# Performance work log

Measured on AMD Instinct MI355X. Metric: run time of the kernel, lower is better.

## Reference

```python
import jax, jax.numpy as jnp
import numpy as np

B, S, D, H, L, OUT = 4, 1024, 1024, 16, 6, 512
HD = D // H
EPS = 1e-5


def _positional_encoding(seq, dim):
    pos = np.arange(seq, dtype=np.float32)[:, None]          # [S,1]
    i = np.arange(0, dim, 2, dtype=np.float32)[None, :]       # even indices
    div = np.power(10000.0, 2.0 * i / dim)                    # repo's (nonstandard) exponent
    pe = np.zeros((seq, dim), dtype=np.float32)
    pe[:, 0::2] = np.sin(pos / div)
    pe[:, 1::2] = np.cos(pos / div)
    return jnp.asarray(pe)[None]                               # [1,S,D]


def _causal_mask(seq):
    r = jnp.arange(seq)
    m = jnp.where(r[None, :] > r[:, None], jnp.float32(-jnp.inf), jnp.float32(0.0))
    return m[None, None]                                       # [1,1,S,S]


def setup_inputs() -> dict:
    key = jax.random.key(0)
    ks = jax.random.split(key, 10)
    sc = 0.02
    inp = {
        'x':      jax.random.normal(ks[0], (B, S, D), jnp.float32),
        'pe':     _positional_encoding(S, D),
        'mask':   _causal_mask(S),
        'ln1_g':  jnp.ones((L, D), jnp.float32),
        'ln1_b':  jnp.zeros((L, D), jnp.float32),
        'wq':     jax.random.normal(ks[1], (L, D, D), jnp.float32) * sc,
        'wk':     jax.random.normal(ks[2], (L, D, D), jnp.float32) * sc,
        'wv':     jax.random.normal(ks[3], (L, D, D), jnp.float32) * sc,
        'wo':     jax.random.normal(ks[4], (L, D, D), jnp.float32) * sc,
        'ln2_g':  jnp.ones((L, D), jnp.float32),
        'ln2_b':  jnp.zeros((L, D), jnp.float32),
        'wf':     jax.random.normal(ks[5], (L, D, D), jnp.float32) * sc,
        'lnf_g':  jnp.ones((D,), jnp.float32),
        'lnf_b':  jnp.zeros((D,), jnp.float32),
        'w_out':  jax.random.normal(ks[6], (OUT, D), jnp.float32) * sc,
    }
    return inp


def _layer_norm(x, g, b):
    mu = jnp.mean(x, axis=-1, keepdims=True)
    var = jnp.mean(jnp.square(x - mu), axis=-1, keepdims=True)
    return (x - mu) * jax.lax.rsqrt(var + EPS) * g + b


def _split_heads(x):
    b, s, d = x.shape
    return x.reshape(b, s, H, HD).transpose(0, 2, 1, 3)  # [B,H,S,HD]


def reference(x, pe, mask, ln1_g, ln1_b, wq, wk, wv, wo, ln2_g, ln2_b, wf, lnf_g, lnf_b, w_out):
    h = x + pe
    scale = 1.0 / jnp.sqrt(jnp.float32(HD))
    for l in range(wq.shape[0]):
        h_ = _layer_norm(h, ln1_g[l], ln1_b[l])
        q = _split_heads(jnp.einsum('bsd,ed->bse', h_, wq[l]))
        k = _split_heads(jnp.einsum('bsd,ed->bse', h_, wk[l]))
        v = _split_heads(jnp.einsum('bsd,ed->bse', h_, wv[l]))
        scores = jnp.einsum('bhqd,bhkd->bhqk', q, k) * scale + mask  # [B,H,S,S]
        probs = jax.nn.softmax(scores, axis=-1)
        attn = jnp.einsum('bhqk,bhkd->bhqd', probs, v)
        attn = attn.transpose(0, 2, 1, 3).reshape(h.shape)            # combine heads
        h = h + jnp.einsum('bsd,ed->bse', attn, wo[l])
        h_ = _layer_norm(h, ln2_g[l], ln2_b[l])
        h = h + jnp.einsum('bsd,ed->bse', h_, wf[l])                  # FFN = plain linear (no activation, as in source)
    h = _layer_norm(h, lnf_g, lnf_b)
    return jnp.einsum('bsd,od->bso', h, w_out)
```

## Files before the change

kernel.cpp:

```cpp
#include <hip/hip_runtime.h>
#include <hip/hip_bf16.h>
#include <stdint.h>

#define BATCH 4
#define SEQ   1024
#define DIM   1024
#define NH    16
#define HDIM  64
#define NLAYER 6
#define NOUT  512
#define NTOK  (BATCH*SEQ)
#define LOG2E 1.44269504088896f
#define NEG_BIG (-1e30f)
#define VTS   72

using bf16 = __hip_bfloat16;
typedef __attribute__((ext_vector_type(4))) float f32x4;
typedef __attribute__((ext_vector_type(8))) short bf16x8;

typedef __attribute__((address_space(1))) void as1_void;
typedef __attribute__((address_space(3))) void as3_void;

__device__ __forceinline__ float bf2f(short u) {
  union { unsigned int i; float f; } c;
  c.i = ((unsigned int)(unsigned short)u) << 16;
  return c.f;
}

__device__ __forceinline__ short f2bs(float f) {
  bf16 h = __float2bfloat16(f);
  return *(short*)&h;
}

__device__ __forceinline__ float exp_clamped(float x) {
  return exp2f(fmaxf(x, -100.f) * LOG2E);
}

__device__ __forceinline__ float loadf(const void* p, size_t i, bool f32) {
  return f32 ? ((const float*)p)[i] : __bfloat162float(((const bf16*)p)[i]);
}

__device__ __forceinline__ void g2l16(const void* g, void* l) {
  __builtin_amdgcn_global_load_lds((const as1_void*)g, (as3_void*)l, 16, 0, 0);
}

__global__ void sniff(const unsigned int* __restrict__ w, int* __restrict__ flag) {
  const int lane = threadIdx.x;
  const unsigned int word = w[lane];
  const int e2 = (word >> 7) & 0xFF;
  const bool bf16ish = (e2 >= 0x60) && (e2 <= 0x8F);
  const unsigned long long m = __ballot(bf16ish);
  if (lane == 0) *flag = (__popcll(m) >= 48) ? 0 : 1;
}

__global__ __launch_bounds__(256) void convert_all(
    const float* __restrict__ s0, const float* __restrict__ s1,
    const float* __restrict__ s2, const float* __restrict__ s3,
    const float* __restrict__ s4, const float* __restrict__ s5,
    bf16* __restrict__ d0, bf16* __restrict__ d1, bf16* __restrict__ d2,
    bf16* __restrict__ d3, bf16* __restrict__ d4, bf16* __restrict__ d5,
    const int* __restrict__ flag) {
  if (*flag == 0) return;
  int b = blockIdx.x;
  const float* s; bf16* d;
  if      (b <  768) { s = s0; d = d0; }
  else if (b < 1536) { s = s1; d = d1; b -= 768; }
  else if (b < 2304) { s = s2; d = d2; b -= 1536; }
  else if (b < 3072) { s = s3; d = d3; b -= 2304; }
  else if (b < 3840) { s = s4; d = d4; b -= 3072; }
  else               { s = s5; d = d5; b -= 3840; }
  const size_t e0 = ((size_t)b * 1024 + threadIdx.x) * 8;
  f32x4 a[4], c[4];
#pragma unroll
  for (int i = 0; i < 4; ++i) {
    a[i] = *(const f32x4*)(s + e0 + i * 2048);
    c[i] = *(const f32x4*)(s + e0 + i * 2048 + 4);
  }
#pragma unroll
  for (int i = 0; i < 4; ++i) {
    bf16x8 o;
    o[0] = f2bs(a[i][0]); o[1] = f2bs(a[i][1]); o[2] = f2bs(a[i][2]); o[3] = f2bs(a[i][3]);
    o[4] = f2bs(c[i][0]); o[5] = f2bs(c[i][1]); o[6] = f2bs(c[i][2]); o[7] = f2bs(c[i][3]);
    *(bf16x8*)(d + e0 + i * 2048) = o;
  }
}

__device__ __forceinline__ bf16x8 rd_frag(const short* panel, int row, int quad) {
  const int g  = row >> 1;
  const int cc = (((row & 1) << 2) | quad) ^ (g & 7);
  return *(const bf16x8*)(panel + g * 64 + cc * 8);
}

template<int EPI>
__device__ __forceinline__ void gemm_body(const bf16* __restrict__ A,
                                          const bf16* __restrict__ W,
                                          void* __restrict__ C,
                                          const int* __restrict__ flag,
                                          int N, int m0, int n0) {
  __shared__ __align__(16) short lA[8192];
  __shared__ __align__(16) short lB[8192];
  const int tid  = threadIdx.x;
  const int wave = tid >> 6;
  const int lane = tid & 63;
  const int quad = lane >> 4;
  const int l16  = lane & 15;
  const int wm = (wave >> 1) * 64;
  const int wn = (wave & 1) * 64;
  const int K = DIM;

  const int c3   = (lane & 7) ^ (lane >> 3);
  const int sq   = (c3 & 3) * 8;
  const int rsub = ((lane >> 3) << 1) | (c3 >> 2);
  const int ldsW = wave * 512;

  bool f32out = false;
  if (EPI == 2) f32out = (*flag != 0);

  f32x4 acc[4][4];
#pragma unroll
  for (int i = 0; i < 4; ++i)
#pragma unroll
    for (int j = 0; j < 4; ++j) acc[i][j] = (f32x4){0.f, 0.f, 0.f, 0.f};

  for (int k0 = 0; k0 < K; k0 += 64) {
    __syncthreads();
#pragma unroll
    for (int kc = 0; kc < 2; ++kc)
#pragma unroll
      for (int c = 0; c < 2; ++c) {
        const int row = c * 64 + wave * 16 + rsub;
        g2l16(A + (size_t)(m0 + row) * K + k0 + kc * 32 + sq,
              lA + kc * 4096 + c * 2048 + ldsW);
        g2l16(W + (size_t)(n0 + row) * K + k0 + kc * 32 + sq,
              lB + kc * 4096 + c * 2048 + ldsW);
      }
    __builtin_amdgcn_s_waitcnt(0);
    __syncthreads();

#pragma unroll
    for (int kc = 0; kc < 2; ++kc) {
      const short* pA = lA + kc * 4096;
      const short* pB = lB + kc * 4096;
      bf16x8 af[4], bfr[4];
#pragma unroll
      for (int i = 0; i < 4; ++i) {
        af[i]  = rd_frag(pA, wm + i * 16 + l16, quad);
        bfr[i] = rd_frag(pB, wn + i * 16 + l16, quad);
      }
#pragma unroll
      for (int i = 0; i < 4; ++i)
#pragma unroll
        for (int j = 0; j < 4; ++j)
          acc[i][j] = __builtin_amdgcn_mfma_f32_16x16x32_bf16(af[i], bfr[j], acc[i][j], 0, 0, 0);
    }
  }

#pragma unroll
  for (int i = 0; i < 4; ++i) {
    const int rowb = m0 + wm + i * 16 + quad * 4;
#pragma unroll
    for (int j = 0; j < 4; ++j) {
      const int col = n0 + wn + j * 16 + l16;
#pragma unroll
      for (int r = 0; r < 4; ++r) {
        const size_t idx = (size_t)(rowb + r) * N + col;
        const float v = acc[i][j][r];
        if (EPI == 0) ((bf16*)C)[idx] = __float2bfloat16(v);
        else { if (f32out) ((float*)C)[idx] = v; else ((bf16*)C)[idx] = __float2bfloat16(v); }
      }
    }
  }
}

__global__ __launch_bounds__(256) void gemm_out(const bf16* __restrict__ A,
                                                const bf16* __restrict__ Wc,
                                                const bf16* __restrict__ Wo,
                                                void* __restrict__ C,
                                                const int* __restrict__ flag) {
  const bf16* W = (*flag != 0) ? Wc : Wo;
  gemm_body<2>(A, W, C, flag, NOUT, blockIdx.y * 128, blockIdx.x * 128);
}

__global__ __launch_bounds__(256) void gemm_qkv(const bf16* __restrict__ A,
                                                const bf16* __restrict__ cq,
                                                const bf16* __restrict__ ck,
                                                const bf16* __restrict__ cvv,
                                                const bf16* __restrict__ oq,
                                                const bf16* __restrict__ ok,
                                                const bf16* __restrict__ ov,
                                                bf16* __restrict__ q,
                                                bf16* __restrict__ k,
                                                bf16* __restrict__ v,
                                                const int* __restrict__ flag) {
  const int gx = blockIdx.x;
  const int sel = gx >> 3;
  const int n0 = (gx & 7) * 128;
  const bool f32 = (*flag != 0);
  const bf16* W = (sel == 0) ? (f32 ? cq : oq)
                 : (sel == 1) ? (f32 ? ck : ok)
                              : (f32 ? cvv : ov);
  bf16* C = (sel == 0) ? q : (sel == 1 ? k : v);
  gemm_body<0>(A, W, C, nullptr, DIM, blockIdx.y * 128, n0);
}

__device__ __forceinline__ void gemm64_body(const bf16* __restrict__ A,
                                            const bf16* __restrict__ W,
                                            float* __restrict__ C,
                                            int N, int m0, int n0) {
  __shared__ __align__(16) short lA[4096];
  __shared__ __align__(16) short lB[8192];
  const int tid  = threadIdx.x;
  const int wave = tid >> 6;
  const int lane = tid & 63;
  const int quad = lane >> 4;
  const int l16  = lane & 15;
  const int wm = (wave >> 1) * 32;
  const int wn = (wave & 1) * 64;
  const int K = DIM;

  const int c3   = (lane & 7) ^ (lane >> 3);
  const int sq   = (c3 & 3) * 8;
  const int rsub = ((lane >> 3) << 1) | (c3 >> 2);
  const int ldsW = wave * 512;

  f32x4 acc[2][4];
#pragma unroll
  for (int i = 0; i < 2; ++i)
#pragma unroll
    for (int j = 0; j < 4; ++j) acc[i][j] = (f32x4){0.f, 0.f, 0.f, 0.f};

  for (int k0 = 0; k0 < K; k0 += 64) {
    __syncthreads();
#pragma unroll
    for (int kc = 0; kc < 2; ++kc) {
      const int arow = wave * 16 + rsub;
      g2l16(A + (size_t)(m0 + arow) * K + k0 + kc * 32 + sq,
            lA + kc * 2048 + ldsW);
#pragma unroll
      for (int c = 0; c < 2; ++c) {
        const int brow = c * 64 + wave * 16 + rsub;
        g2l16(W + (size_t)(n0 + brow) * K + k0 + kc * 32 + sq,
              lB + kc * 4096 + c * 2048 + ldsW);
      }
    }
    __builtin_amdgcn_s_waitcnt(0);
    __syncthreads();

#pragma unroll
    for (int kc = 0; kc < 2; ++kc) {
      const short* pA = lA + kc * 2048;
      const short* pB = lB + kc * 4096;
      bf16x8 af[2], bfr[4];
#pragma unroll
      for (int i = 0; i < 2; ++i)
        af[i] = rd_frag(pA, wm + i * 16 + l16, quad);
#pragma unroll
      for (int j = 0; j < 4; ++j)
        bfr[j] = rd_frag(pB, wn + j * 16 + l16, quad);
#pragma unroll
      for (int i = 0; i < 2; ++i)
#pragma unroll
        for (int j = 0; j < 4; ++j)
          acc[i][j] = __builtin_amdgcn_mfma_f32_16x16x32_bf16(af[i], bfr[j], acc[i][j], 0, 0, 0);
    }
  }

#pragma unroll
  for (int i = 0; i < 2; ++i) {
    const int rowb = m0 + wm + i * 16 + quad * 4;
#pragma unroll
    for (int j = 0; j < 4; ++j) {
      const int col = n0 + wn + j * 16 + l16;
#pragma unroll
      for (int r = 0; r < 4; ++r)
        C[(size_t)(rowb + r) * N + col] += acc[i][j][r];
    }
  }
}

__global__ __launch_bounds__(256) void gemm_add(const bf16* __restrict__ A,
                                                const bf16* __restrict__ Wc,
                                                const bf16* __restrict__ Wo,
                                                const int* __restrict__ flag,
                                                float* __restrict__ C) {
  const bf16* W = (*flag != 0) ? Wc : Wo;
  gemm64_body(A, W, C, DIM, blockIdx.y * 64, blockIdx.x * 128);
}

__global__ __launch_bounds__(256) void add_pe(const void* __restrict__ x,
                                              const void* __restrict__ pe,
                                              float* __restrict__ h,
                                              const int* __restrict__ flag) {
  const bool f32 = (*flag != 0);
  const size_t i = (size_t)blockIdx.x * 256 + threadIdx.x;
  h[i] = loadf(x, i, f32) + loadf(pe, i & (SEQ * DIM - 1), f32);
}

__global__ __launch_bounds__(256) void layernorm(const float* __restrict__ x,
                                                 const void* __restrict__ g,
                                                 const void* __restrict__ b,
                                                 int loff,
                                                 bf16* __restrict__ y,
                                                 const int* __restrict__ flag) {
  const bool f32 = (*flag != 0);
  const int row = blockIdx.x;
  const int tid = threadIdx.x;
  const int wave = tid >> 6;
  const float* xr = x + (size_t)row * DIM;
  __shared__ float red[8];

  float v[4];
  float s = 0.f;
#pragma unroll
  for (int i = 0; i < 4; ++i) { v[i] = xr[tid + 256 * i]; s += v[i]; }
#pragma unroll
  for (int off = 32; off >= 1; off >>= 1) s += __shfl_xor(s, off);
  if ((tid & 63) == 0) red[wave] = s;
  __syncthreads();
  const float mu = (red[0] + red[1] + red[2] + red[3]) * (1.f / DIM);

  float vs = 0.f;
#pragma unroll
  for (int i = 0; i < 4; ++i) { const float d = v[i] - mu; vs += d * d; }
#pragma unroll
  for (int off = 32; off >= 1; off >>= 1) vs += __shfl_xor(vs, off);
  if ((tid & 63) == 0) red[4 + wave] = vs;
  __syncthreads();
  const float var = (red[4] + red[5] + red[6] + red[7]) * (1.f / DIM);
  const float rs = rsqrtf(var + 1e-5f);

#pragma unroll
  for (int i = 0; i < 4; ++i) {
    const int d = tid + 256 * i;
    const float gv = loadf(g, (size_t)loff + d, f32);
    const float bv = loadf(b, (size_t)loff + d, f32);
    y[(size_t)row * DIM + d] = __float2bfloat16((v[i] - mu) * rs * gv + bv);
  }
}

__global__ __launch_bounds__(256, 2) void attn_flash(const bf16* __restrict__ q,
                                                     const bf16* __restrict__ k,
                                                     const bf16* __restrict__ v,
                                                     bf16* __restrict__ o) {
  __shared__ __align__(16) short lK[64 * 64];
  __shared__ __align__(16) short lVT[64 * VTS];
  __shared__ __align__(16) short lP[4 * 16 * VTS];

  const int idx = blockIdx.x;
  const int qt = (SEQ / 64 - 1) - (idx >> 6);
  const int bh = idx & 63;
  const int hh = bh & (NH - 1);
  const int bb = bh >> 4;
  const int q0 = qt * 64;

  const int tid = threadIdx.x;
  const int wave = tid >> 6;
  const int lane = tid & 63;
  const int quad = lane >> 4;
  const int l16 = lane & 15;

  const size_t base = (size_t)bb * SEQ * DIM + hh * HDIM;
  const int qlo = q0 + wave * 16;

  bf16x8 qf[2];
  {
    const bf16* qr = q + base + (size_t)(qlo + l16) * DIM;
#pragma unroll
    for (int kc = 0; kc < 2; ++kc) {
      bf16x8 t = *(const bf16x8*)(qr + kc * 32 + quad * 8);
      bf16x8 sq;
#pragma unroll
      for (int e = 0; e < 8; ++e) sq[e] = f2bs(bf2f(t[e]) * 0.125f);
      qf[kc] = sq;
    }
  }

  float l_acc[4] = {0.f, 0.f, 0.f, 0.f};
  f32x4 oacc[4];
#pragma unroll
  for (int nb = 0; nb < 4; ++nb) oacc[nb] = (f32x4){0.f, 0.f, 0.f, 0.f};

  short* lPw = lP + wave * 16 * VTS;
  const int nt = qt + 1;

  for (int t = 0; t < nt; ++t) {
    const int kbase = t * 64;
    __syncthreads();

    {
      const int r8 = lane >> 3;
      const int cc = (lane & 7) ^ r8;
#pragma unroll
      for (int c = 0; c < 2; ++c) {
        const int row = wave * 16 + c * 8 + r8;
        g2l16(k + base + (size_t)(kbase + row) * DIM + cc * 8,
              lK + (wave * 16 + c * 8) * 64);
      }
    }

    bf16x8 vch[2];
#pragma unroll
    for (int c2 = 0; c2 < 2; ++c2) {
      const int cid = tid + c2 * 256;
      const int kk = cid >> 3;
      const int d0 = (cid & 7) * 8;
      vch[c2] = *(const bf16x8*)(v + base + (size_t)(kbase + kk) * DIM + d0);
    }
#pragma unroll
    for (int c2 = 0; c2 < 2; ++c2) {
      const int cid = tid + c2 * 256;
      const int kk = cid >> 3;
      const int d0 = (cid & 7) * 8;
#pragma unroll
      for (int e = 0; e < 8; ++e) {
        const int d = d0 + e;
        const int kks = kk ^ (((d >> 3) & 7) << 3);
        lVT[d * VTS + kks] = vch[c2][e];
      }
    }
    __builtin_amdgcn_s_waitcnt(0);
    __syncthreads();

    f32x4 s[4];
#pragma unroll
    for (int nb = 0; nb < 4; ++nb) {
      f32x4 acc = (f32x4){0.f, 0.f, 0.f, 0.f};
      const int n = nb * 16 + l16;
#pragma unroll
      for (int kc = 0; kc < 2; ++kc) {
        const int cidx = (kc * 4 + quad) ^ (n & 7);
        bf16x8 kf = *(const bf16x8*)(lK + n * 64 + cidx * 8);
        acc = __builtin_amdgcn_mfma_f32_16x16x32_bf16(qf[kc], kf, acc, 0, 0, 0);
      }
      s[nb] = acc;
    }

    if (kbase + 63 > qlo) {
#pragma unroll
      for (int nb = 0; nb < 4; ++nb) {
        const int j = kbase + nb * 16 + l16;
#pragma unroll
        for (int r = 0; r < 4; ++r)
          if (j > qlo + quad * 4 + r) s[nb][r] = NEG_BIG;
      }
    }

#pragma unroll
    for (int nb = 0; nb < 4; ++nb) {
#pragma unroll
      for (int r = 0; r < 4; ++r) {
        const float p = exp_clamped(s[nb][r]);
        l_acc[r] += p;
        lPw[(quad * 4 + r) * VTS + nb * 16 + l16] = f2bs(p);
      }
    }

    __builtin_amdgcn_s_waitcnt(0);
    bf16x8 pf[2];
#pragma unroll
    for (int kc = 0; kc < 2; ++kc)
      pf[kc] = *(const bf16x8*)(lPw + l16 * VTS + kc * 32 + quad * 8);

#pragma unroll
    for (int nb = 0; nb < 4; ++nb) {
      const int n = nb * 16 + l16;
      const int swz = ((n >> 3) & 7) << 3;
#pragma unroll
      for (int kc = 0; kc < 2; ++kc) {
        const int kchunk = (kc * 32 + quad * 8) ^ swz;
        bf16x8 vf = *(const bf16x8*)(lVT + n * VTS + kchunk);
        oacc[nb] = __builtin_amdgcn_mfma_f32_16x16x32_bf16(pf[kc], vf, oacc[nb], 0, 0, 0);
      }
    }
  }

  float linv[4];
#pragma unroll
  for (int r = 0; r < 4; ++r) {
    float ts = l_acc[r];
#pragma unroll
    for (int off = 8; off >= 1; off >>= 1) ts += __shfl_xor(ts, off);
    linv[r] = 1.f / ts;
  }
#pragma unroll
  for (int nb = 0; nb < 4; ++nb)
#pragma unroll
    for (int r = 0; r < 4; ++r) {
      const int qrow = q0 + wave * 16 + quad * 4 + r;
      o[base + (size_t)qrow * DIM + nb * 16 + l16] =
          __float2bfloat16(oacc[nb][r] * linv[r]);
    }
}

extern "C" void kernel_launch(void* const* d_in, const int* in_sizes, int n_in,
                              void* d_out, int out_size, void* d_ws, size_t ws_size,
                              hipStream_t stream) {
  const void* x    = d_in[0];
  const void* pe   = d_in[1];
  const void* ln1g = d_in[3];
  const void* ln1b = d_in[4];
  const void* wq   = d_in[5];
  const void* wk   = d_in[6];
  const void* wv   = d_in[7];
  const void* wo   = d_in[8];
  const void* ln2g = d_in[9];
  const void* ln2b = d_in[10];
  const void* wf   = d_in[11];
  const void* lnfg = d_in[12];
  const void* lnfb = d_in[13];
  const void* wout = d_in[14];

  const size_t MB = 1u << 20;
  char* ws = (char*)d_ws;
  int*  flag = (int*)ws;
  bf16* wqc  = (bf16*)(ws + 1 * MB);
  bf16* wkc  = (bf16*)(ws + 13 * MB);
  bf16* wvc  = (bf16*)(ws + 25 * MB);
  bf16* woc  = (bf16*)(ws + 37 * MB);
  bf16* wfc  = (bf16*)(ws + 49 * MB);
  bf16* woutc= (bf16*)(ws + 61 * MB);
  float* h   = (float*)(ws + 62 * MB);
  bf16* hn   = (bf16*)(ws + 78 * MB);
  bf16* qb   = (bf16*)(ws + 86 * MB);
  bf16* kb   = (bf16*)(ws + 94 * MB);
  bf16* vb   = (bf16*)(ws + 102 * MB);
  bf16* ab   = hn;

  sniff<<<1, 64, 0, stream>>>((const unsigned int*)wq, flag);

  convert_all<<<3904, 256, 0, stream>>>(
      (const float*)wq, (const float*)wk, (const float*)wv,
      (const float*)wo, (const float*)wf, (const float*)wout,
      wqc, wkc, wvc, woc, wfc, woutc, flag);

  add_pe<<<NTOK * DIM / 256, 256, 0, stream>>>(x, pe, h, flag);

  for (int l = 0; l < NLAYER; ++l) {
    const size_t woff = (size_t)l << 20;
    const int poff = l * DIM;
    layernorm<<<NTOK, 256, 0, stream>>>(h, ln1g, ln1b, poff, hn, flag);
    gemm_qkv<<<dim3(24, 32), 256, 0, stream>>>(
        hn, wqc + woff, wkc + woff, wvc + woff,
        (const bf16*)wq + woff, (const bf16*)wk + woff, (const bf16*)wv + woff,
        qb, kb, vb, flag);
    attn_flash<<<dim3(BATCH * NH * (SEQ / 64)), 256, 0, stream>>>(qb, kb, vb, ab);
    gemm_add<<<dim3(8, 64), 256, 0, stream>>>(ab, woc + woff,
                                              (const bf16*)wo + woff, flag, h);
    layernorm<<<NTOK, 256, 0, stream>>>(h, ln2g, ln2b, poff, hn, flag);
    gemm_add<<<dim3(8, 64), 256, 0, stream>>>(hn, wfc + woff,
                                              (const bf16*)wf + woff, flag, h);
  }

  layernorm<<<NTOK, 256, 0, stream>>>(h, lnfg, lnfb, 0, hn, flag);
  gemm_out<<<dim3(4, 32), 256, 0, stream>>>(hn, woutc, (const bf16*)wout,
                                            d_out, flag);
}
```

Before: 914.0 us.

## Process two KV tiles per sync in attention, vectorize add_pe, smaller output GEMM tiles

The flash attention loop now stages two 64-key K/V tiles per barrier pair, halving the number of __syncthreads and letting the global loads for both tiles overlap, at the cost of doubled LDS usage. add_pe is vectorized to four elements per thread. The final output projection switches to the 64-row GEMM body, doubling its block count so more CUs are busy for the small 4096x512 output. Higher LDS per block may reduce attention occupancy.

Measured after the change: 906.9 us. About the same (-0.8%).

```diff
diff --git a/kernel.cpp b/kernel.cpp
--- a/kernel.cpp
+++ b/kernel.cpp
@@ -17,6 +17,7 @@
 using bf16 = __hip_bfloat16;
 typedef __attribute__((ext_vector_type(4))) float f32x4;
 typedef __attribute__((ext_vector_type(8))) short bf16x8;
+typedef __attribute__((ext_vector_type(4))) short bf16x4;
 
 typedef __attribute__((address_space(1))) void as1_void;
 typedef __attribute__((address_space(3))) void as3_void;
@@ -170,15 +171,6 @@
       }
     }
   }
-}
-
-__global__ __launch_bounds__(256) void gemm_out(const bf16* __restrict__ A,
-                                                const bf16* __restrict__ Wc,
-                                                const bf16* __restrict__ Wo,
-                                                void* __restrict__ C,
-                                                const int* __restrict__ flag) {
-  const bf16* W = (*flag != 0) ? Wc : Wo;
-  gemm_body<2>(A, W, C, flag, NOUT, blockIdx.y * 128, blockIdx.x * 128);
 }
 
 __global__ __launch_bounds__(256) void gemm_qkv(const bf16* __restrict__ A,
@@ -203,9 +195,11 @@
   gemm_body<0>(A, W, C, nullptr, DIM, blockIdx.y * 128, n0);
 }
 
+template<int EPI>
 __device__ __forceinline__ void gemm64_body(const bf16* __restrict__ A,
                                             const bf16* __restrict__ W,
-                                            float* __restrict__ C,
+                                            void* __restrict__ C,
+                                            const int* __restrict__ flag,
                                             int N, int m0, int n0) {
   __shared__ __align__(16) short lA[4096];
   __shared__ __align__(16) short lB[8192];
@@ -223,6 +217,9 @@
   const int rsub = ((lane >> 3) << 1) | (c3 >> 2);
   const int ldsW = wave * 512;
 
+  bool f32out = false;
+  if (EPI == 2) f32out = (*flag != 0);
+
   f32x4 acc[2][4];
 #pragma unroll
   for (int i = 0; i < 2; ++i)
@@ -272,8 +269,12 @@
     for (int j = 0; j < 4; ++j) {
       const int col = n0 + wn + j * 16 + l16;
 #pragma unroll
-      for (int r = 0; r < 4; ++r)
-        C[(size_t)(rowb + r) * N + col] += acc[i][j][r];
+      for (int r = 0; r < 4; ++r) {
+        const size_t idx = (size_t)(rowb + r) * N + col;
+        const float v = acc[i][j][r];
+        if (EPI == 0) ((float*)C)[idx] += v;
+        else { if (f32out) ((float*)C)[idx] = v; else ((bf16*)C)[idx] = __float2bfloat16(v); }
+      }
     }
   }
 }
@@ -284,7 +285,16 @@
                                                 const int* __restrict__ flag,
                                                 float* __restrict__ C) {
   const bf16* W = (*flag != 0) ? Wc : Wo;
-  gemm64_body(A, W, C, DIM, blockIdx.y * 64, blockIdx.x * 128);
+  gemm64_body<0>(A, W, C, nullptr, DIM, blockIdx.y * 64, blockIdx.x * 128);
+}
+
+__global__ __launch_bounds__(256) void gemm_out(const bf16* __restrict__ A,
+                                                const bf16* __restrict__ Wc,
+                                                const bf16* __restrict__ Wo,
+                                                void* __restrict__ C,
+                                                const int* __restrict__ flag) {
+  const bf16* W = (*flag != 0) ? Wc : Wo;
+  gemm64_body<2>(A, W, C, flag, NOUT, blockIdx.y * 64, blockIdx.x * 128);
 }
 
 __global__ __launch_bounds__(256) void add_pe(const void* __restrict__ x,
@@ -292,8 +302,21 @@
                                               float* __restrict__ h,
                                               const int* __restrict__ flag) {
   const bool f32 = (*flag != 0);
-  const size_t i = (size_t)blockIdx.x * 256 + threadIdx.x;
-  h[i] = loadf(x, i, f32) + loadf(pe, i & (SEQ * DIM - 1), f32);
+  const size_t i = ((size_t)blockIdx.x * 256 + threadIdx.x) * 4;
+  const size_t p = i & (SEQ * DIM - 1);
+  f32x4 r;
+  if (f32) {
+    const f32x4 xv = *(const f32x4*)((const float*)x + i);
+    const f32x4 pv = *(const f32x4*)((const float*)pe + p);
+#pragma unroll
+    for (int e = 0; e < 4; ++e) r[e] = xv[e] + pv[e];
+  } else {
+    const bf16x4 xv = *(const bf16x4*)((const bf16*)x + i);
+    const bf16x4 pv = *(const bf16x4*)((const bf16*)pe + p);
+#pragma unroll
+    for (int e = 0; e < 4; ++e) r[e] = bf2f(xv[e]) + bf2f(pv[e]);
+  }
+  *(f32x4*)(h + i) = r;
 }
 
 __global__ __launch_bounds__(256) void layernorm(const float* __restrict__ x,
@@ -342,8 +365,8 @@
                                                      const bf16* __restrict__ k,
                                                      const bf16* __restrict__ v,
                                                      bf16* __restrict__ o) {
-  __shared__ __align__(16) short lK[64 * 64];
-  __shared__ __align__(16) short lVT[64 * VTS];
+  __shared__ __align__(16) short lK[2 * 64 * 64];
+  __shared__ __align__(16) short lVT[2 * 64 * VTS];
   __shared__ __align__(16) short lP[4 * 16 * VTS];
 
   const int idx = blockIdx.x;
@@ -383,93 +406,119 @@
   short* lPw = lP + wave * 16 * VTS;
   const int nt = qt + 1;
 
-  for (int t = 0; t < nt; ++t) {
-    const int kbase = t * 64;
+  for (int t0 = 0; t0 < nt; t0 += 2) {
     __syncthreads();
 
     {
       const int r8 = lane >> 3;
       const int cc = (lane & 7) ^ r8;
 #pragma unroll
-      for (int c = 0; c < 2; ++c) {
-        const int row = wave * 16 + c * 8 + r8;
-        g2l16(k + base + (size_t)(kbase + row) * DIM + cc * 8,
-              lK + (wave * 16 + c * 8) * 64);
-      }
-    }
-
-    bf16x8 vch[2];
-#pragma unroll
-    for (int c2 = 0; c2 < 2; ++c2) {
-      const int cid = tid + c2 * 256;
-      const int kk = cid >> 3;
-      const int d0 = (cid & 7) * 8;
-      vch[c2] = *(const bf16x8*)(v + base + (size_t)(kbase + kk) * DIM + d0);
-    }
-#pragma unroll
-    for (int c2 = 0; c2 < 2; ++c2) {
-      const int cid = tid + c2 * 256;
-      const int kk = cid >> 3;
-      const int d0 = (cid & 7) * 8;
-#pragma unroll
-      for (int e = 0; e < 8; ++e) {
-        const int d = d0 + e;
-        const int kks = kk ^ (((d >> 3) & 7) << 3);
-        lVT[d * VTS + kks] = vch[c2][e];
+      for (int h2 = 0; h2 < 2; ++h2) {
+        if (t0 + h2 < nt) {
+          const int kbase = (t0 + h2) * 64;
+#pragma unroll
+          for (int c = 0; c < 2; ++c) {
+            const int row = wave * 16 + c * 8 + r8;
+            g2l16(k + base + (size_t)(kbase + row) * DIM + cc * 8,
+                  lK + h2 * 4096 + (wave * 16 + c * 8) * 64);
+          }
+        }
+      }
+    }
+
+    bf16x8 vch[2][2];
+#pragma unroll
+    for (int h2 = 0; h2 < 2; ++h2) {
+      if (t0 + h2 < nt) {
+        const int kbase = (t0 + h2) * 64;
+#pragma unroll
+        for (int c2 = 0; c2 < 2; ++c2) {
+          const int cid = tid + c2 * 256;
+          const int kk = cid >> 3;
+          const int d0 = (cid & 7) * 8;
+          vch[h2][c2] = *(const bf16x8*)(v + base + (size_t)(kbase + kk) * DIM + d0);
+        }
+      }
+    }
+#pragma unroll
+    for (int h2 = 0; h2 < 2; ++h2) {
+      if (t0 + h2 < nt) {
+#pragma unroll
+        for (int c2 = 0; c2 < 2; ++c2) {
+          const int cid = tid + c2 * 256;
+          const int kk = cid >> 3;
+          const int d0 = (cid & 7) * 8;
+#pragma unroll
+          for (int e = 0; e < 8; ++e) {
+            const int d = d0 + e;
+            const int kks = kk ^ (((d >> 3) & 7) << 3);
+            lVT[h2 * 64 * VTS + d * VTS + kks] = vch[h2][c2][e];
+          }
+        }
       }
     }
     __builtin_amdgcn_s_waitcnt(0);
     __syncthreads();
 
-    f32x4 s[4];
-#pragma unroll
-    for (int nb = 0; nb < 4; ++nb) {
-      f32x4 acc = (f32x4){0.f, 0.f, 0.f, 0.f};
-      const int n = nb * 16 + l16;
-#pragma unroll
-      for (int kc = 0; kc < 2; ++kc) {
-        const int cidx = (kc * 4 + quad) ^ (n & 7);
-        bf16x8 kf = *(const bf16x8*)(lK + n * 64 + cidx * 8);
-        acc = __builtin_amdgcn_mfma_f32_16x16x32_bf16(qf[kc], kf, acc, 0, 0, 0);
-      }
-      s[nb] = acc;
-    }
-
-    if (kbase + 63 > qlo) {
-#pragma unroll
-      for (int nb = 0; nb < 4; ++nb) {
-        const int j = kbase + nb * 16 + l16;
-#pragma unroll
-        for (int r = 0; r < 4; ++r)
-          if (j > qlo + quad * 4 + r) s[nb][r] = NEG_BIG;
-      }
-    }
-
-#pragma unroll
-    for (int nb = 0; nb < 4; ++nb) {
-#pragma unroll
-      for (int r = 0; r < 4; ++r) {
-        const float p = exp_clamped(s[nb][r]);
-        l_acc[r] += p;
-        lPw[(quad * 4 + r) * VTS + nb * 16 + l16] = f2bs(p);
-      }
-    }
-
-    __builtin_amdgcn_s_waitcnt(0);
-    bf16x8 pf[2];
-#pragma unroll
-    for (int kc = 0; kc < 2; ++kc)
-      pf[kc] = *(const bf16x8*)(lPw + l16 * VTS + kc * 32 + quad * 8);
-
-#pragma unroll
-    for (int nb = 0; nb < 4; ++nb) {
-      const int n = nb * 16 + l16;
-      const int swz = ((n >> 3) & 7) << 3;
-#pragma unroll
-      for (int kc = 0; kc < 2; ++kc) {
-        const int kchunk = (kc * 32 + quad * 8) ^ swz;
-        bf16x8 vf = *(const bf16x8*)(lVT + n * VTS + kchunk);
-        oacc[nb] = __builtin_amdgcn_mfma_f32_16x16x32_bf16(pf[kc], vf, oacc[nb], 0, 0, 0);
+#pragma unroll
+    for (int h2 = 0; h2 < 2; ++h2) {
+      const int t = t0 + h2;
+      if (t < nt) {
+        const int kbase = t * 64;
+        const short* lKh = lK + h2 * 4096;
+        const short* lVh = lVT + h2 * 64 * VTS;
+
+        f32x4 s[4];
+#pragma unroll
+        for (int nb = 0; nb < 4; ++nb) {
+          f32x4 acc = (f32x4){0.f, 0.f, 0.f, 0.f};
+          const int n = nb * 16 + l16;
+#pragma unroll
+          for (int kc = 0; kc < 2; ++kc) {
+            const int cidx = (kc * 4 + quad) ^ (n & 7);
+            bf16x8 kf = *(const bf16x8*)(lKh + n * 64 + cidx * 8);
+            acc = __builtin_amdgcn_mfma_f32_16x16x32_bf16(qf[kc], kf, acc, 0, 0, 0);
+          }
+          s[nb] = acc;
+        }
+
+        if (kbase + 63 > qlo) {
+#pragma unroll
+          for (int nb = 0; nb < 4; ++nb) {
+            const int j = kbase + nb * 16 + l16;
+#pragma unroll
+            for (int r = 0; r < 4; ++r)
+              if (j > qlo + quad * 4 + r) s[nb][r] = NEG_BIG;
+          }
+        }
+
+#pragma unroll
+        for (int nb = 0; nb < 4; ++nb) {
+#pragma unroll
+          for (int r = 0; r < 4; ++r) {
+            const float p = exp_clamped(s[nb][r]);
+            l_acc[r] += p;
+            lPw[(quad * 4 + r) * VTS + nb * 16 + l16] = f2bs(p);
+          }
+        }
+
+        __builtin_amdgcn_s_waitcnt(0);
+        bf16x8 pf[2];
+#pragma unroll
+        for (int kc = 0; kc < 2; ++kc)
+          pf[kc] = *(const bf16x8*)(lPw + l16 * VTS + kc * 32 + quad * 8);
+
+#pragma unroll
+        for (int nb = 0; nb < 4; ++nb) {
+          const int n = nb * 16 + l16;
+          const int swz = ((n >> 3) & 7) << 3;
+#pragma unroll
+          for (int kc = 0; kc < 2; ++kc) {
+            const int kchunk = (kc * 32 + quad * 8) ^ swz;
+            bf16x8 vf = *(const bf16x8*)(lVh + n * VTS + kchunk);
+            oacc[nb] = __builtin_amdgcn_mfma_f32_16x16x32_bf16(pf[kc], vf, oacc[nb], 0, 0, 0);
+          }
+        }
       }
     }
   }
@@ -533,7 +582,7 @@
       (const float*)wo, (const float*)wf, (const float*)wout,
       wqc, wkc, wvc, woc, wfc, woutc, flag);
 
-  add_pe<<<NTOK * DIM / 256, 256, 0, stream>>>(x, pe, h, flag);
+  add_pe<<<NTOK * DIM / (256 * 4), 256, 0, stream>>>(x, pe, h, flag);
 
   for (int l = 0; l < NLAYER; ++l) {
     const size_t woff = (size_t)l << 20;
@@ -552,6 +601,6 @@
   }
 
   layernorm<<<NTOK, 256, 0, stream>>>(h, lnfg, lnfb, 0, hn, flag);
-  gemm_out<<<dim3(4, 32), 256, 0, stream>>>(hn, woutc, (const bf16*)wout,
+  gemm_out<<<dim3(4, 64), 256, 0, stream>>>(hn, woutc, (const bf16*)wout,
                                             d_out, flag);
 }
```
